# Performance work log

Measured on AMD Instinct MI355X. Metric: run time of the kernel, lower is better.

Reference implementation:

```python
import jax, jax.numpy as jnp
import numpy as np

N, C, T, V = 128, 256, 48, 25
CR = C // 16
SEG = 3
BN_EPS = 1e-5


def setup_inputs() -> dict:
    key = jax.random.key(0)
    ks = jax.random.split(key, 8)
    s = lambda k, shape: jax.random.normal(k, shape, dtype=jnp.float32) * 0.05
    return {
        "x": jax.random.normal(ks[0], (N, C, T, V), dtype=jnp.float32),
        "w_sq": s(ks[1], (CR, C)),   # me_squeeze 1x1 conv weight [out,in]
        "b_sq": s(ks[2], (CR,)),
        "gamma": jnp.ones((CR,), jnp.float32),   # BN weight
        "beta": jnp.zeros((CR,), jnp.float32),   # BN bias
        "rmean": jnp.zeros((CR,), jnp.float32),  # BN running mean
        "rvar": jnp.ones((CR,), jnp.float32),    # BN running var
        "w_c1": s(ks[3], (CR, CR)),  # me_conv1 1x1 conv weight
        "b_c1": s(ks[4], (CR,)),
        "w_ex": s(ks[5], (C, CR)),   # me_expand 1x1 conv weight
        "b_ex": s(ks[6], (C,)),
    }


def reference(x, w_sq, b_sq, gamma, beta, rmean, rvar, w_c1, b_c1, w_ex, b_ex):
    n, c, t, v = x.shape
    nb = (n * t) // SEG
    cr = w_sq.shape[0]
    # 1x1 squeeze conv + BatchNorm (eval mode, running stats) -> [n, cr, t, v]
    y = jnp.einsum('nctv,rc->nrtv', x, w_sq) + b_sq[None, :, None, None]
    scale = gamma / jnp.sqrt(rvar + BN_EPS)
    y = y * scale[None, :, None, None] + (beta - rmean * scale)[None, :, None, None]
    # 1x1 conv on squeezed features (shifted branch)
    y1 = jnp.einsum('nrtv,sr->nstv', y, w_c1) + b_c1[None, :, None, None]
    # regroup consecutive frames into segments of SEG along time: (n*t) -> (nb, SEG)
    yseg = y.transpose(0, 2, 1, 3).reshape(nb, SEG, cr, v)
    y1seg = y1.transpose(0, 2, 1, 3).reshape(nb, SEG, cr, v)
    # temporal difference: conv(frame k+1) - frame k, zero-pad last frame of each segment
    diff = y1seg[:, 1:] - yseg[:, :SEG - 1]                    # [nb, SEG-1, cr, v]
    diff = jnp.pad(diff, ((0, 0), (0, 1), (0, 0), (0, 0)))     # [nb, SEG, cr, v]
    x_me = diff.reshape(n, t, cr, v).transpose(0, 2, 1, 3)     # [n, cr, t, v]
    # adaptive avg pool over joints (v -> 1), expand conv, sigmoid gate
    m = jnp.mean(x_me, axis=-1, keepdims=True)                 # [n, cr, t, 1]
    gate = jax.nn.sigmoid(jnp.einsum('nrtu,cr->nctu', m, w_ex) + b_ex[None, :, None, None])
    return x * gate
```

## Files before the change

### kernel.cpp

```cpp
#include <hip/hip_runtime.h>
#include <hip/hip_bf16.h>

#define N_  128
#define C_  256
#define T_  48
#define V_  25

__device__ __forceinline__ float b2f(unsigned short u) {
    union { float f; unsigned i; } c; c.i = ((unsigned)u) << 16; return c.f;
}
__device__ __forceinline__ unsigned short f2b(float f) {
    __hip_bfloat16 h = __float2bfloat16(f);
    return *(unsigned short*)&h;
}

__global__ __launch_bounds__(512, 4) void k_fused2(
    const float* __restrict__ x,
    const float* __restrict__ wsq, const float* __restrict__ bsq,
    const float* __restrict__ gamma, const float* __restrict__ beta,
    const float* __restrict__ rmean, const float* __restrict__ rvar,
    const float* __restrict__ wc1, const float* __restrict__ bc1,
    const float* __restrict__ wex, const float* __restrict__ bex,
    float* __restrict__ out)
{
    __shared__ __align__(16) unsigned short sbuf[64 * 300];
    __shared__ float xb[256 * 12];
    __shared__ float part[384];
    __shared__ float ybn[192];
    __shared__ float y1[192];
    __shared__ float mv[192];
    __shared__ float gs[256 * 12];

    const int tid = threadIdx.x;
    const unsigned bid = blockIdx.x;
    const unsigned o   = (bid & 7u) * 64u + (bid >> 3);
    const unsigned n   = o >> 2;
    const unsigned sg  = o & 3u;

    const float* xg = x   + (size_t)n * 307200u + sg * 300u;
    float*       og = out + (size_t)n * 307200u + sg * 300u;

    for (int cg = 0; cg < 4; ++cg) {
        for (int it = 0; it < 10; ++it) {
            int j = it * 512 + tid;
            if (j < 4800) {
                int cl  = j / 75;
                int pos = j - cl * 75;
                const float4 v = *(const float4*)(xg + (unsigned)(cg * 64 + cl) * 1200u + (unsigned)pos * 4u);
                ushort4 u;
                u.x = f2b(v.x); u.y = f2b(v.y); u.z = f2b(v.z); u.w = f2b(v.w);
                *(ushort4*)(sbuf + j * 4) = u;
            }
        }
        __syncthreads();
        for (int p = tid; p < 768; p += 512) {
            int cl = p / 12, t = p - cl * 12;
            const unsigned short* row = sbuf + cl * 300 + t * 25;
            float s = 0.f;
            #pragma unroll
            for (int v = 0; v < 25; ++v) s += b2f(row[v]);
            xb[(cg * 64 + cl) * 12 + t] = s * (1.f / 25.f);
        }
        __syncthreads();
    }

    if (tid < 384) {
        int t = tid >> 5;
        int rh = tid & 31;
        int r = rh >> 1, h = rh & 1;
        const float* wrow = wsq + r * 256 + h * 128;
        float acc = 0.f;
        #pragma unroll 8
        for (int i = 0; i < 128; ++i) acc += xb[(h * 128 + i) * 12 + t] * wrow[i];
        part[tid] = acc;
    }
    __syncthreads();
    if (tid < 192) {
        int t = tid >> 4, r = tid & 15;
        float acc = part[t * 32 + r * 2] + part[t * 32 + r * 2 + 1];
        float sc = gamma[r] * rsqrtf(rvar[r] + 1e-5f);
        ybn[t * 16 + r] = (acc + bsq[r]) * sc + (beta[r] - rmean[r] * sc);
    }
    __syncthreads();
    if (tid < 192) {
        int t = tid >> 4, s = tid & 15;
        float acc = bc1[s];
        #pragma unroll
        for (int r = 0; r < 16; ++r) acc += ybn[t * 16 + r] * wc1[s * 16 + r];
        y1[t * 16 + s] = acc;
    }
    __syncthreads();
    if (tid < 192) {
        int t = tid >> 4, r = tid & 15;
        mv[tid] = ((t % 3) < 2) ? (y1[(t + 1) * 16 + r] - ybn[t * 16 + r]) : 0.f;
    }
    __syncthreads();
    {
        int c = tid & 255, th = tid >> 8;
        float wexr[16];
        #pragma unroll
        for (int r = 0; r < 16; ++r) wexr[r] = wex[c * 16 + r];
        float be = bex[c];
        for (int t = th * 6; t < th * 6 + 6; ++t) {
            float a = be;
            #pragma unroll
            for (int r = 0; r < 16; ++r) a += mv[t * 16 + r] * wexr[r];
            gs[c * 12 + t] = 1.f / (1.f + expf(-a));
        }
    }
    __syncthreads();

    for (int it = 0; it < 38; ++it) {
        int j = it * 512 + tid;
        if (j < 19200) {
            int c = j / 75, pos = j - c * 75;
            const float4 v = *(const float4*)(xg + (unsigned)c * 1200u + (unsigned)pos * 4u);
            int p4  = pos * 4;
            int t0  = p4 / 25;
            int t3  = (p4 + 3) / 25;
            int rem = p4 - t0 * 25;
            float g0 = gs[c * 12 + t0];
            float g3 = gs[c * 12 + t3];
            float4 ov;
            ov.x = v.x * g0;
            ov.y = v.y * ((rem + 1 < 25) ? g0 : g3);
            ov.z = v.z * ((rem + 2 < 25) ? g0 : g3);
            ov.w = v.w * ((rem + 3 < 25) ? g0 : g3);
            *(float4*)(og + (unsigned)c * 1200u + (unsigned)pos * 4u) = ov;
        }
    }
}

extern "C" void kernel_launch(void* const* d_in, const int* in_sizes, int n_in,
                              void* d_out, int out_size, void* d_ws, size_t ws_size,
                              hipStream_t stream) {
    const float* x     = (const float*)d_in[0];
    const float* wsq   = (const float*)d_in[1];
    const float* bsq   = (const float*)d_in[2];
    const float* gamma = (const float*)d_in[3];
    const float* beta  = (const float*)d_in[4];
    const float* rmean = (const float*)d_in[5];
    const float* rvar  = (const float*)d_in[6];
    const float* wc1   = (const float*)d_in[7];
    const float* bc1   = (const float*)d_in[8];
    const float* wex   = (const float*)d_in[9];
    const float* bex   = (const float*)d_in[10];

    k_fused2<<<512, 512, 0, stream>>>(x, wsq, bsq, gamma, beta,
                                      rmean, rvar, wc1, bc1, wex, bex,
                                      (float*)d_out);
}
```

Before: 92.01 us.

## Split work into half-size time segments and pool directly from registers

Each block now handles 6 frames (two 3-frame segments) instead of 12, which doubles the grid to 1024 blocks and raises the occupancy hint to 8. The bf16 shared-memory staging buffer is dropped: each thread loads 7 float4 of one channel/frame row and sums its 25 joints in registers. The gating pass switches to float2 accesses with a multiply-shift frame index. These changes aim to reduce shared-memory footprint and synchronisation and improve parallelism, at the cost of redundant and misaligned overlapping loads and narrower vector stores.

```diff
diff --git a/kernel.cpp b/kernel.cpp
--- a/kernel.cpp
+++ b/kernel.cpp
@@ -1,20 +1,11 @@
 #include <hip/hip_runtime.h>
-#include <hip/hip_bf16.h>
 
 #define N_  128
 #define C_  256
 #define T_  48
 #define V_  25
 
-__device__ __forceinline__ float b2f(unsigned short u) {
-    union { float f; unsigned i; } c; c.i = ((unsigned)u) << 16; return c.f;
-}
-__device__ __forceinline__ unsigned short f2b(float f) {
-    __hip_bfloat16 h = __float2bfloat16(f);
-    return *(unsigned short*)&h;
-}
-
-__global__ __launch_bounds__(512, 4) void k_fused2(
+__global__ __launch_bounds__(512, 8) void k_fused3(
     const float* __restrict__ x,
     const float* __restrict__ wsq, const float* __restrict__ bsq,
     const float* __restrict__ gamma, const float* __restrict__ beta,
@@ -23,66 +14,63 @@
     const float* __restrict__ wex, const float* __restrict__ bex,
     float* __restrict__ out)
 {
-    __shared__ __align__(16) unsigned short sbuf[64 * 300];
-    __shared__ float xb[256 * 12];
-    __shared__ float part[384];
-    __shared__ float ybn[192];
-    __shared__ float y1[192];
-    __shared__ float mv[192];
-    __shared__ float gs[256 * 12];
+    __shared__ float xb[256 * 6];
+    __shared__ float part[192];
+    __shared__ float ybn[96];
+    __shared__ float y1[96];
+    __shared__ float mv[96];
+    __shared__ float gs[256 * 6];
 
     const int tid = threadIdx.x;
     const unsigned bid = blockIdx.x;
-    const unsigned o   = (bid & 7u) * 64u + (bid >> 3);
-    const unsigned n   = o >> 2;
-    const unsigned sg  = o & 3u;
+    const unsigned o   = (bid & 7u) * 128u + (bid >> 3);
+    const unsigned n   = o >> 3;
+    const unsigned sg2 = o & 7u;
 
-    const float* xg = x   + (size_t)n * 307200u + sg * 300u;
-    float*       og = out + (size_t)n * 307200u + sg * 300u;
+    const size_t nbase = (size_t)n * 307200u;
+    const unsigned soff = sg2 * 150u;
 
-    for (int cg = 0; cg < 4; ++cg) {
-        for (int it = 0; it < 10; ++it) {
-            int j = it * 512 + tid;
-            if (j < 4800) {
-                int cl  = j / 75;
-                int pos = j - cl * 75;
-                const float4 v = *(const float4*)(xg + (unsigned)(cg * 64 + cl) * 1200u + (unsigned)pos * 4u);
-                ushort4 u;
-                u.x = f2b(v.x); u.y = f2b(v.y); u.z = f2b(v.z); u.w = f2b(v.w);
-                *(ushort4*)(sbuf + j * 4) = u;
-            }
+    #pragma unroll
+    for (int k = 0; k < 3; ++k) {
+        int f  = k * 512 + tid;
+        int c  = f / 6;
+        int tl = f - c * 6;
+        int off = (int)soff + c * 1200 + tl * 25;
+        int mis = off & 3;
+        const float4* p = (const float4*)(x + nbase + (unsigned)(off - mis));
+        float w[28];
+        #pragma unroll
+        for (int q = 0; q < 7; ++q) {
+            float4 v = p[q];
+            w[4*q] = v.x; w[4*q+1] = v.y; w[4*q+2] = v.z; w[4*q+3] = v.w;
         }
-        __syncthreads();
-        for (int p = tid; p < 768; p += 512) {
-            int cl = p / 12, t = p - cl * 12;
-            const unsigned short* row = sbuf + cl * 300 + t * 25;
-            float s = 0.f;
-            #pragma unroll
-            for (int v = 0; v < 25; ++v) s += b2f(row[v]);
-            xb[(cg * 64 + cl) * 12 + t] = s * (1.f / 25.f);
-        }
-        __syncthreads();
+        float s = 0.f;
+        #pragma unroll
+        for (int i = 3; i <= 24; ++i) s += w[i];
+        s += (mis == 0) ? w[0] : w[25];
+        s += (mis <= 1) ? w[1] : w[26];
+        s += (mis <= 2) ? w[2] : w[27];
+        xb[f] = s * 0.04f;
     }
+    __syncthreads();
 
-    if (tid < 384) {
-        int t = tid >> 5;
-        int rh = tid & 31;
-        int r = rh >> 1, h = rh & 1;
+    if (tid < 192) {
+        int t = tid >> 5, rh = tid & 31, r = rh >> 1, h = rh & 1;
         const float* wrow = wsq + r * 256 + h * 128;
         float acc = 0.f;
         #pragma unroll 8
-        for (int i = 0; i < 128; ++i) acc += xb[(h * 128 + i) * 12 + t] * wrow[i];
+        for (int i = 0; i < 128; ++i) acc += xb[(h * 128 + i) * 6 + t] * wrow[i];
         part[tid] = acc;
     }
     __syncthreads();
-    if (tid < 192) {
+    if (tid < 96) {
         int t = tid >> 4, r = tid & 15;
         float acc = part[t * 32 + r * 2] + part[t * 32 + r * 2 + 1];
         float sc = gamma[r] * rsqrtf(rvar[r] + 1e-5f);
         ybn[t * 16 + r] = (acc + bsq[r]) * sc + (beta[r] - rmean[r] * sc);
     }
     __syncthreads();
-    if (tid < 192) {
+    if (tid < 96) {
         int t = tid >> 4, s = tid & 15;
         float acc = bc1[s];
         #pragma unroll
@@ -90,7 +78,7 @@
         y1[t * 16 + s] = acc;
     }
     __syncthreads();
-    if (tid < 192) {
+    if (tid < 96) {
         int t = tid >> 4, r = tid & 15;
         mv[tid] = ((t % 3) < 2) ? (y1[(t + 1) * 16 + r] - ybn[t * 16 + r]) : 0.f;
     }
@@ -101,32 +89,32 @@
         #pragma unroll
         for (int r = 0; r < 16; ++r) wexr[r] = wex[c * 16 + r];
         float be = bex[c];
-        for (int t = th * 6; t < th * 6 + 6; ++t) {
+        #pragma unroll
+        for (int t = th * 3; t < th * 3 + 3; ++t) {
             float a = be;
             #pragma unroll
             for (int r = 0; r < 16; ++r) a += mv[t * 16 + r] * wexr[r];
-            gs[c * 12 + t] = 1.f / (1.f + expf(-a));
+            gs[c * 6 + t] = 1.f / (1.f + expf(-a));
         }
     }
     __syncthreads();
 
+    const float* xg = x   + nbase + soff;
+    float*       og = out + nbase + soff;
+    #pragma unroll 4
     for (int it = 0; it < 38; ++it) {
         int j = it * 512 + tid;
         if (j < 19200) {
-            int c = j / 75, pos = j - c * 75;
-            const float4 v = *(const float4*)(xg + (unsigned)c * 1200u + (unsigned)pos * 4u);
-            int p4  = pos * 4;
-            int t0  = p4 / 25;
-            int t3  = (p4 + 3) / 25;
-            int rem = p4 - t0 * 25;
-            float g0 = gs[c * 12 + t0];
-            float g3 = gs[c * 12 + t3];
-            float4 ov;
-            ov.x = v.x * g0;
-            ov.y = v.y * ((rem + 1 < 25) ? g0 : g3);
-            ov.z = v.z * ((rem + 2 < 25) ? g0 : g3);
-            ov.w = v.w * ((rem + 3 < 25) ? g0 : g3);
-            *(float4*)(og + (unsigned)c * 1200u + (unsigned)pos * 4u) = ov;
+            int c  = j / 75;
+            int p2 = j - c * 75;
+            int e0 = p2 * 2;
+            int t0 = (e0 * 41) >> 10;
+            int t1 = ((e0 + 1) * 41) >> 10;
+            float2 v = *(const float2*)(xg + (unsigned)(c * 1200 + e0));
+            float2 ov;
+            ov.x = v.x * gs[c * 6 + t0];
+            ov.y = v.y * gs[c * 6 + t1];
+            *(float2*)(og + (unsigned)(c * 1200 + e0)) = ov;
         }
     }
 }
@@ -146,7 +134,7 @@
     const float* wex   = (const float*)d_in[9];
     const float* bex   = (const float*)d_in[10];
 
-    k_fused2<<<512, 512, 0, stream>>>(x, wsq, bsq, gamma, beta,
-                                      rmean, rvar, wc1, bc1, wex, bex,
-                                      (float*)d_out);
+    k_fused3<<<1024, 512, 0, stream>>>(x, wsq, bsq, gamma, beta,
+                                       rmean, rvar, wc1, bc1, wex, bex,
+                                       (float*)d_out);
 }
```

New measurement: 95.66 us. 4.0% more time.

## Reduce joint means directly from registers, dropping bf16 LDS staging

Applied to the files above, without the earlier changes.

The first pass no longer converts x to bf16 and stages it in shared memory in four synchronized channel groups. Each thread now loads seven aligned float4s covering one (channel, frame) row of 25 joints, picks out the 25 valid values according to the row's misalignment, and writes the mean straight to xb. This removes the LDS round trip and most of the barriers, and computes the means in fp32 instead of bf16. The second pass adds an unroll hint and replaces the divide by 25 with a multiply-shift. The cost is higher register pressure and somewhat redundant, partly overlapping global loads.

```diff
diff --git a/kernel.cpp b/kernel.cpp
--- a/kernel.cpp
+++ b/kernel.cpp
@@ -1,20 +1,11 @@
 #include <hip/hip_runtime.h>
-#include <hip/hip_bf16.h>
 
 #define N_  128
 #define C_  256
 #define T_  48
 #define V_  25
 
-__device__ __forceinline__ float b2f(unsigned short u) {
-    union { float f; unsigned i; } c; c.i = ((unsigned)u) << 16; return c.f;
-}
-__device__ __forceinline__ unsigned short f2b(float f) {
-    __hip_bfloat16 h = __float2bfloat16(f);
-    return *(unsigned short*)&h;
-}
-
-__global__ __launch_bounds__(512, 4) void k_fused2(
+__global__ __launch_bounds__(512, 4) void k_fused4(
     const float* __restrict__ x,
     const float* __restrict__ wsq, const float* __restrict__ bsq,
     const float* __restrict__ gamma, const float* __restrict__ beta,
@@ -23,7 +14,6 @@
     const float* __restrict__ wex, const float* __restrict__ bex,
     float* __restrict__ out)
 {
-    __shared__ __align__(16) unsigned short sbuf[64 * 300];
     __shared__ float xb[256 * 12];
     __shared__ float part[384];
     __shared__ float ybn[192];
@@ -40,34 +30,42 @@
     const float* xg = x   + (size_t)n * 307200u + sg * 300u;
     float*       og = out + (size_t)n * 307200u + sg * 300u;
 
-    for (int cg = 0; cg < 4; ++cg) {
-        for (int it = 0; it < 10; ++it) {
-            int j = it * 512 + tid;
-            if (j < 4800) {
-                int cl  = j / 75;
-                int pos = j - cl * 75;
-                const float4 v = *(const float4*)(xg + (unsigned)(cg * 64 + cl) * 1200u + (unsigned)pos * 4u);
-                ushort4 u;
-                u.x = f2b(v.x); u.y = f2b(v.y); u.z = f2b(v.z); u.w = f2b(v.w);
-                *(ushort4*)(sbuf + j * 4) = u;
-            }
+    #pragma unroll
+    for (int kk = 0; kk < 3; ++kk) {
+        const int fA = (2 * kk) * 512 + tid;
+        const int fB = (2 * kk + 1) * 512 + tid;
+        const int cA = fA / 12, tA = fA - cA * 12;
+        const int cB = fB / 12, tB = fB - cB * 12;
+        const int misA = (tA * 25) & 3, misB = (tB * 25) & 3;
+        const float4* pA = (const float4*)(xg + (unsigned)(cA * 1200 + tA * 25 - misA));
+        const float4* pB = (const float4*)(xg + (unsigned)(cB * 1200 + tB * 25 - misB));
+        float4 va[7], vb[7];
+        #pragma unroll
+        for (int q = 0; q < 7; ++q) va[q] = pA[q];
+        #pragma unroll
+        for (int q = 0; q < 7; ++q) vb[q] = pB[q];
+        float wa[28], wb[28];
+        #pragma unroll
+        for (int q = 0; q < 7; ++q) {
+            wa[4*q] = va[q].x; wa[4*q+1] = va[q].y; wa[4*q+2] = va[q].z; wa[4*q+3] = va[q].w;
+            wb[4*q] = vb[q].x; wb[4*q+1] = vb[q].y; wb[4*q+2] = vb[q].z; wb[4*q+3] = vb[q].w;
         }
-        __syncthreads();
-        for (int p = tid; p < 768; p += 512) {
-            int cl = p / 12, t = p - cl * 12;
-            const unsigned short* row = sbuf + cl * 300 + t * 25;
-            float s = 0.f;
-            #pragma unroll
-            for (int v = 0; v < 25; ++v) s += b2f(row[v]);
-            xb[(cg * 64 + cl) * 12 + t] = s * (1.f / 25.f);
-        }
-        __syncthreads();
+        float sA = 0.f, sB = 0.f;
+        #pragma unroll
+        for (int i = 3; i <= 24; ++i) { sA += wa[i]; sB += wb[i]; }
+        sA += (misA == 0) ? wa[0] : wa[25];
+        sA += (misA <= 1) ? wa[1] : wa[26];
+        sA += (misA <= 2) ? wa[2] : wa[27];
+        sB += (misB == 0) ? wb[0] : wb[25];
+        sB += (misB <= 1) ? wb[1] : wb[26];
+        sB += (misB <= 2) ? wb[2] : wb[27];
+        xb[fA] = sA * 0.04f;
+        xb[fB] = sB * 0.04f;
     }
+    __syncthreads();
 
     if (tid < 384) {
-        int t = tid >> 5;
-        int rh = tid & 31;
-        int r = rh >> 1, h = rh & 1;
+        int t = tid >> 5, rh = tid & 31, r = rh >> 1, h = rh & 1;
         const float* wrow = wsq + r * 256 + h * 128;
         float acc = 0.f;
         #pragma unroll 8
@@ -101,6 +99,7 @@
         #pragma unroll
         for (int r = 0; r < 16; ++r) wexr[r] = wex[c * 16 + r];
         float be = bex[c];
+        #pragma unroll
         for (int t = th * 6; t < th * 6 + 6; ++t) {
             float a = be;
             #pragma unroll
@@ -110,14 +109,15 @@
     }
     __syncthreads();
 
+    #pragma unroll 4
     for (int it = 0; it < 38; ++it) {
         int j = it * 512 + tid;
         if (j < 19200) {
             int c = j / 75, pos = j - c * 75;
-            const float4 v = *(const float4*)(xg + (unsigned)c * 1200u + (unsigned)pos * 4u);
+            const float4 v = *(const float4*)(xg + (unsigned)(c * 1200 + pos * 4));
             int p4  = pos * 4;
-            int t0  = p4 / 25;
-            int t3  = (p4 + 3) / 25;
+            int t0  = (p4 * 41) >> 10;
+            int t3  = ((p4 + 3) * 41) >> 10;
             int rem = p4 - t0 * 25;
             float g0 = gs[c * 12 + t0];
             float g3 = gs[c * 12 + t3];
@@ -126,7 +126,7 @@
             ov.y = v.y * ((rem + 1 < 25) ? g0 : g3);
             ov.z = v.z * ((rem + 2 < 25) ? g0 : g3);
             ov.w = v.w * ((rem + 3 < 25) ? g0 : g3);
-            *(float4*)(og + (unsigned)c * 1200u + (unsigned)pos * 4u) = ov;
+            *(float4*)(og + (unsigned)(c * 1200 + pos * 4)) = ov;
         }
     }
 }
@@ -146,7 +146,7 @@
     const float* wex   = (const float*)d_in[9];
     const float* bex   = (const float*)d_in[10];
 
-    k_fused2<<<512, 512, 0, stream>>>(x, wsq, bsq, gamma, beta,
+    k_fused4<<<512, 512, 0, stream>>>(x, wsq, bsq, gamma, beta,
                                       rmean, rvar, wc1, bc1, wex, bex,
                                       (float*)d_out);
 }
```

Result: no change. 92.54 us (+0.6%).

## Replace staged bf16 pooling with single-pass LDS atomic pooling and transposed weights

Applied to the files above, without the earlier changes.

Drops the four-pass bf16 staging buffer and its per-group barriers. Each float4 of x is now reduced straight into per-(channel,time) sums with LDS atomicAdd in one pass. The squeeze weights are staged transposed and padded in LDS, the gate-expand weights are loaded early, the 1/25 mean is folded into the BN scale, and output stores become nontemporal. LDS atomics can contend on shared bins, and the change also removes the bf16 rounding of x.

```diff
diff --git a/kernel.cpp b/kernel.cpp
--- a/kernel.cpp
+++ b/kernel.cpp
@@ -1,20 +1,13 @@
 #include <hip/hip_runtime.h>
-#include <hip/hip_bf16.h>
 
 #define N_  128
 #define C_  256
 #define T_  48
 #define V_  25
 
-__device__ __forceinline__ float b2f(unsigned short u) {
-    union { float f; unsigned i; } c; c.i = ((unsigned)u) << 16; return c.f;
-}
-__device__ __forceinline__ unsigned short f2b(float f) {
-    __hip_bfloat16 h = __float2bfloat16(f);
-    return *(unsigned short*)&h;
-}
+typedef float v4f __attribute__((ext_vector_type(4)));
 
-__global__ __launch_bounds__(512, 4) void k_fused2(
+__global__ __launch_bounds__(512, 4) void k_fused6(
     const float* __restrict__ x,
     const float* __restrict__ wsq, const float* __restrict__ bsq,
     const float* __restrict__ gamma, const float* __restrict__ beta,
@@ -23,63 +16,76 @@
     const float* __restrict__ wex, const float* __restrict__ bex,
     float* __restrict__ out)
 {
-    __shared__ __align__(16) unsigned short sbuf[64 * 300];
     __shared__ float xb[256 * 12];
-    __shared__ float part[384];
+    __shared__ float wsqL[256 * 17];
+    __shared__ float gs[256 * 12];
     __shared__ float ybn[192];
     __shared__ float y1[192];
     __shared__ float mv[192];
-    __shared__ float gs[256 * 12];
 
     const int tid = threadIdx.x;
     const unsigned bid = blockIdx.x;
-    const unsigned o   = (bid & 7u) * 64u + (bid >> 3);
-    const unsigned n   = o >> 2;
-    const unsigned sg  = o & 3u;
+    const unsigned o = (bid & 7u) * 64u + (bid >> 3);
+    const unsigned n = o >> 2;
+    const unsigned q = o & 3u;
 
-    const float* xg = x   + (size_t)n * 307200u + sg * 300u;
-    float*       og = out + (size_t)n * 307200u + sg * 300u;
+    const unsigned base4 = n * 76800u + q * 75u;
+    const v4f* x4 = (const v4f*)x;
+    v4f*       o4 = (v4f*)out;
 
-    for (int cg = 0; cg < 4; ++cg) {
-        for (int it = 0; it < 10; ++it) {
-            int j = it * 512 + tid;
-            if (j < 4800) {
-                int cl  = j / 75;
-                int pos = j - cl * 75;
-                const float4 v = *(const float4*)(xg + (unsigned)(cg * 64 + cl) * 1200u + (unsigned)pos * 4u);
-                ushort4 u;
-                u.x = f2b(v.x); u.y = f2b(v.y); u.z = f2b(v.z); u.w = f2b(v.w);
-                *(ushort4*)(sbuf + j * 4) = u;
+    #pragma unroll
+    for (int j = tid; j < 3072; j += 512) xb[j] = 0.f;
+    #pragma unroll
+    for (int it = 0; it < 8; ++it) {
+        int j = it * 512 + tid;
+        int r = j >> 8, c = j & 255;
+        wsqL[c * 17 + r] = wsq[j];
+    }
+    float wexr[16];
+    #pragma unroll
+    for (int r = 0; r < 16; ++r) wexr[r] = wex[(tid & 255) * 16 + r];
+    const float bexr = bex[tid & 255];
+    __syncthreads();
+
+    for (int it = 0; it < 38; ++it) {
+        int j = it * 512 + tid;
+        if (j < 19200) {
+            int c = j / 75, k = j - c * 75;
+            v4f v = x4[base4 + (unsigned)(c * 300 + k)];
+            int m0 = k * 4;
+            int t0 = (m0 * 41) >> 10;
+            int t3 = ((m0 + 3) * 41) >> 10;
+            float s = (v.x + v.y) + (v.z + v.w);
+            if (t0 == t3) {
+                atomicAdd(&xb[c * 12 + t0], s);
+            } else {
+                int r = 25 - (m0 - t0 * 25);
+                float sA = v.x + ((r > 1) ? v.y : 0.f) + ((r > 2) ? v.z : 0.f);
+                atomicAdd(&xb[c * 12 + t0], sA);
+                atomicAdd(&xb[c * 12 + t3], s - sA);
             }
         }
-        __syncthreads();
-        for (int p = tid; p < 768; p += 512) {
-            int cl = p / 12, t = p - cl * 12;
-            const unsigned short* row = sbuf + cl * 300 + t * 25;
-            float s = 0.f;
-            #pragma unroll
-            for (int v = 0; v < 25; ++v) s += b2f(row[v]);
-            xb[(cg * 64 + cl) * 12 + t] = s * (1.f / 25.f);
-        }
-        __syncthreads();
     }
+    __syncthreads();
 
     if (tid < 384) {
-        int t = tid >> 5;
-        int rh = tid & 31;
-        int r = rh >> 1, h = rh & 1;
-        const float* wrow = wsq + r * 256 + h * 128;
+        int r = tid & 15, tq = tid >> 4;
+        int t = (tq >= 12) ? tq - 12 : tq;
+        int g = (tq >= 12) ? 1 : 0;
         float acc = 0.f;
         #pragma unroll 8
-        for (int i = 0; i < 128; ++i) acc += xb[(h * 128 + i) * 12 + t] * wrow[i];
-        part[tid] = acc;
+        for (int i = 0; i < 128; ++i) {
+            int c = g * 128 + i;
+            acc += xb[c * 12 + t] * wsqL[c * 17 + r];
+        }
+        gs[tid] = acc;
     }
     __syncthreads();
     if (tid < 192) {
         int t = tid >> 4, r = tid & 15;
-        float acc = part[t * 32 + r * 2] + part[t * 32 + r * 2 + 1];
+        float acc = gs[t * 16 + r] + gs[(t + 12) * 16 + r];
         float sc = gamma[r] * rsqrtf(rvar[r] + 1e-5f);
-        ybn[t * 16 + r] = (acc + bsq[r]) * sc + (beta[r] - rmean[r] * sc);
+        ybn[t * 16 + r] = acc * (0.04f * sc) + (bsq[r] * sc + beta[r] - rmean[r] * sc);
     }
     __syncthreads();
     if (tid < 192) {
@@ -97,12 +103,9 @@
     __syncthreads();
     {
         int c = tid & 255, th = tid >> 8;
-        float wexr[16];
         #pragma unroll
-        for (int r = 0; r < 16; ++r) wexr[r] = wex[c * 16 + r];
-        float be = bex[c];
         for (int t = th * 6; t < th * 6 + 6; ++t) {
-            float a = be;
+            float a = bexr;
             #pragma unroll
             for (int r = 0; r < 16; ++r) a += mv[t * 16 + r] * wexr[r];
             gs[c * 12 + t] = 1.f / (1.f + expf(-a));
@@ -113,20 +116,20 @@
     for (int it = 0; it < 38; ++it) {
         int j = it * 512 + tid;
         if (j < 19200) {
-            int c = j / 75, pos = j - c * 75;
-            const float4 v = *(const float4*)(xg + (unsigned)c * 1200u + (unsigned)pos * 4u);
-            int p4  = pos * 4;
-            int t0  = p4 / 25;
-            int t3  = (p4 + 3) / 25;
-            int rem = p4 - t0 * 25;
+            int c = j / 75, k = j - c * 75;
+            v4f v = x4[base4 + (unsigned)(c * 300 + k)];
+            int m0  = k * 4;
+            int t0  = (m0 * 41) >> 10;
+            int t3  = ((m0 + 3) * 41) >> 10;
+            int rem = m0 - t0 * 25;
             float g0 = gs[c * 12 + t0];
             float g3 = gs[c * 12 + t3];
-            float4 ov;
+            v4f ov;
             ov.x = v.x * g0;
             ov.y = v.y * ((rem + 1 < 25) ? g0 : g3);
             ov.z = v.z * ((rem + 2 < 25) ? g0 : g3);
             ov.w = v.w * ((rem + 3 < 25) ? g0 : g3);
-            *(float4*)(og + (unsigned)c * 1200u + (unsigned)pos * 4u) = ov;
+            __builtin_nontemporal_store(ov, &o4[base4 + (unsigned)(c * 300 + k)]);
         }
     }
 }
@@ -146,7 +149,7 @@
     const float* wex   = (const float*)d_in[9];
     const float* bex   = (const float*)d_in[10];
 
-    k_fused2<<<512, 512, 0, stream>>>(x, wsq, bsq, gamma, beta,
+    k_fused6<<<512, 512, 0, stream>>>(x, wsq, bsq, gamma, beta,
                                       rmean, rvar, wc1, bc1, wex, bex,
                                       (float*)d_out);
 }
```

New measurement: 115.8 us. 25.9% more time.
